# Optimization experiments

Hardware: AMD Instinct MI355X
Metric: run time of the kernel (lower is better)

The kernel has to match this reference:

```python
import jax, jax.numpy as jnp
import numpy as np

MARGIN = 0.5
AP_VALUE = 0.8
AN_VALUE = 0.4
ABS_W = 1.0


def setup_inputs() -> dict:
    key = jax.random.key(0)
    k1, k2 = jax.random.split(key)
    bs, d = 16384, 64
    inputs = jax.random.normal(k1, (bs, d), dtype=jnp.float32)
    target = jax.random.randint(k2, (bs,), 0, 64, dtype=jnp.int64)
    return {"inputs": inputs, "target": target}


def reference(inputs, target):
    # L2-normalize features (normalize_feature=True)
    x = inputs / jnp.linalg.norm(inputs, axis=-1, keepdims=True)

    # cross-entropy on normalized features treated as logits
    logp = jax.nn.log_softmax(x, axis=-1)  # [bs, d]
    loss_ce = -jnp.mean(jnp.take_along_axis(logp, target[:, None], axis=1))

    # cosine-similarity matrix [bs, bs]
    dist = x @ x.T

    is_pos = target[None, :] == target[:, None]
    # hard mining: min similarity among positives, max among negatives (per row)
    dist_ap = jnp.min(jnp.where(is_pos, dist, jnp.inf), axis=1)   # [bs]
    dist_an = jnp.max(jnp.where(is_pos, -jnp.inf, dist), axis=1)  # [bs]

    loss = jnp.mean(jax.nn.relu(MARGIN + dist_ap - dist_an))

    # absolute (angular margin) terms
    abs_ap = jax.nn.relu(AP_VALUE - dist_ap)
    abs_an = jax.nn.relu(dist_an - AN_VALUE)
    loss = (jnp.mean(abs_an) + jnp.mean(abs_ap)) * ABS_W + loss

    return loss + loss_ce
```

## Files before the change

kernel.cpp:

```cpp
#include <hip/hip_runtime.h>


#define N_ROWS 16384
#define N_DIM 64

typedef __attribute__((ext_vector_type(8))) short bf16x8;
typedef __attribute__((ext_vector_type(4))) float f32x4;

__device__ inline unsigned short f2bf(float f) {
  unsigned u = __float_as_uint(f);
  unsigned r = u + 0x7fffu + ((u >> 16) & 1u);
  return (unsigned short)(r >> 16);
}

__device__ inline unsigned enc_key(float f) {
  unsigned u = __float_as_uint(f);
  return (u & 0x80000000u) ? ~u : (u | 0x80000000u);
}
__device__ inline float dec_key(unsigned k) {
  unsigned u = (k & 0x80000000u) ? (k ^ 0x80000000u) : ~k;
  return __uint_as_float(u);
}

__global__ void perm_kernel(const int* __restrict__ tgt, int* __restrict__ perm,
                            int* __restrict__ ts, int* __restrict__ class_start,
                            unsigned* __restrict__ mp_key, unsigned* __restrict__ mn_key) {
  __shared__ int hist[64];
  __shared__ int start[65];
  __shared__ int cursor[64];
  const int tid = threadIdx.x;
  if (tid < 64) hist[tid] = 0;
  for (int i = tid; i < N_ROWS; i += 1024) { mp_key[i] = 0xFFFFFFFFu; mn_key[i] = 0u; }
  __syncthreads();
  int c[16];
#pragma unroll
  for (int k = 0; k < 16; ++k) {
    c[k] = tgt[tid + k * 1024];
    atomicAdd(&hist[c[k]], 1);
  }
  __syncthreads();
  if (tid < 64) {
    int s = 0;
    for (int j = 0; j < tid; ++j) s += hist[j];
    start[tid] = s; cursor[tid] = s; class_start[tid] = s;
    if (tid == 63) { start[64] = s + hist[63]; class_start[64] = s + hist[63]; }
  }
  __syncthreads();
#pragma unroll
  for (int k = 0; k < 16; ++k) {
    const int r = tid + k * 1024;
    const int pos = atomicAdd(&cursor[c[k]], 1);
    perm[r] = pos;
    ts[pos] = c[k];
  }
}

__global__ void prep_kernel(const float* __restrict__ x, const int* __restrict__ tgt,
                            const int* __restrict__ perm,
                            unsigned short* __restrict__ xs, float* __restrict__ ce_row) {
  const int row  = blockIdx.x * 4 + (threadIdx.x >> 6);
  const int lane = threadIdx.x & 63;
  float v  = x[row * N_DIM + lane];
  float ss = v * v;
#pragma unroll
  for (int s = 1; s < 64; s <<= 1) ss += __shfl_xor(ss, s, 64);
  float xn = v * rsqrtf(ss);
  xs[perm[row] * N_DIM + lane] = f2bf(xn);

  float mx = xn;
#pragma unroll
  for (int s = 1; s < 64; s <<= 1) mx = fmaxf(mx, __shfl_xor(mx, s, 64));
  float e  = __expf(xn - mx);
  float se = e;
#pragma unroll
  for (int s = 1; s < 64; s <<= 1) se += __shfl_xor(se, s, 64);
  float lse = mx + __logf(se);
  int   t   = tgt[row];
  float xt  = __shfl(xn, t, 64);
  if (lane == 0) ce_row[row] = lse - xt;
}

__global__ void mine_kernel(const unsigned short* __restrict__ xs, const int* __restrict__ ts,
                            const int* __restrict__ class_start,
                            unsigned* __restrict__ mp_key, unsigned* __restrict__ mn_key) {
  const int lane    = threadIdx.x & 63;
  const int wv      = threadIdx.x >> 6;
  const int iblk    = blockIdx.x >> 5;
  const int jspl    = blockIdx.x & 31;
  const int rowbase = iblk * 256 + wv * 64;
  const int m = lane & 15, q = lane >> 4;

  bf16x8 a[4][2];
#pragma unroll
  for (int tr = 0; tr < 4; ++tr) {
    const unsigned short* p = xs + (rowbase + tr * 16 + m) * N_DIM + q * 8;
    a[tr][0] = *(const bf16x8*)(p);
    a[tr][1] = *(const bf16x8*)(p + 32);
  }
  int ti[4][4];
#pragma unroll
  for (int tr = 0; tr < 4; ++tr)
#pragma unroll
    for (int r = 0; r < 4; ++r)
      ti[tr][r] = ts[rowbase + tr * 16 + q * 4 + r];

  const int cmin = ts[rowbase];
  const int cmax = ts[rowbase + 63];
  const int lo   = class_start[cmin];
  const int hi   = class_start[cmax + 1];

  float mp[16], mn[16];
#pragma unroll
  for (int k = 0; k < 16; ++k) { mp[k] = __builtin_inff(); mn[k] = -__builtin_inff(); }

  const int jbase = jspl * 512;

  const unsigned short* p0 = xs + (jbase + m) * N_DIM + q * 8;
  bf16x8 b0 = *(const bf16x8*)p0;
  bf16x8 b1 = *(const bf16x8*)(p0 + 32);

  for (int jc = 0; jc < 32; ++jc) {
    bf16x8 cb0 = b0, cb1 = b1;
    const int jb = jbase + jc * 16;
    if (jc < 31) {
      const unsigned short* np = xs + (jb + 16 + m) * N_DIM + q * 8;
      b0 = *(const bf16x8*)np;
      b1 = *(const bf16x8*)(np + 32);
    }
    const bool slow = (jb < hi) && (jb + 16 > lo);
    if (slow) {
      const int ctj = ts[jb + m];
#pragma unroll
      for (int tr = 0; tr < 4; ++tr) {
        f32x4 acc = {0.f, 0.f, 0.f, 0.f};
        acc = __builtin_amdgcn_mfma_f32_16x16x32_bf16(a[tr][0], cb0, acc, 0, 0, 0);
        acc = __builtin_amdgcn_mfma_f32_16x16x32_bf16(a[tr][1], cb1, acc, 0, 0, 0);
#pragma unroll
        for (int r = 0; r < 4; ++r) {
          const bool  pos = (ctj == ti[tr][r]);
          const float d   = acc[r];
          const int   k   = tr * 4 + r;
          mp[k] = fminf(mp[k], pos ? d : __builtin_inff());
          mn[k] = fmaxf(mn[k], pos ? -__builtin_inff() : d);
        }
      }
    } else {
#pragma unroll
      for (int tr = 0; tr < 4; ++tr) {
        f32x4 acc = {0.f, 0.f, 0.f, 0.f};
        acc = __builtin_amdgcn_mfma_f32_16x16x32_bf16(a[tr][0], cb0, acc, 0, 0, 0);
        acc = __builtin_amdgcn_mfma_f32_16x16x32_bf16(a[tr][1], cb1, acc, 0, 0, 0);
#pragma unroll
        for (int r = 0; r < 4; ++r)
          mn[tr * 4 + r] = fmaxf(mn[tr * 4 + r], acc[r]);
      }
    }
  }

#pragma unroll
  for (int s = 1; s < 16; s <<= 1) {
#pragma unroll
    for (int k = 0; k < 16; ++k) {
      mp[k] = fminf(mp[k], __shfl_xor(mp[k], s, 64));
      mn[k] = fmaxf(mn[k], __shfl_xor(mn[k], s, 64));
    }
  }
  if (m == 0) {
#pragma unroll
    for (int tr = 0; tr < 4; ++tr)
#pragma unroll
      for (int r = 0; r < 4; ++r) {
        const int row = rowbase + tr * 16 + q * 4 + r;
        atomicMin(&mp_key[row], enc_key(mp[tr * 4 + r]));
        atomicMax(&mn_key[row], enc_key(mn[tr * 4 + r]));
      }
  }
}

__global__ void finalize_kernel(const unsigned* __restrict__ mp_key, const unsigned* __restrict__ mn_key,
                                const float* __restrict__ ce_row, float* __restrict__ out) {
  __shared__ float red[4][16];
  float s1 = 0.f, s2 = 0.f, s3 = 0.f, s4 = 0.f;
  for (int r = threadIdx.x; r < N_ROWS; r += 1024) {
    float ap = dec_key(mp_key[r]);
    float an = dec_key(mn_key[r]);
    s1 += fmaxf(0.5f + ap - an, 0.f);
    s2 += fmaxf(0.8f - ap, 0.f);
    s3 += fmaxf(an - 0.4f, 0.f);
    s4 += ce_row[r];
  }
#pragma unroll
  for (int s = 1; s < 64; s <<= 1) {
    s1 += __shfl_xor(s1, s, 64);
    s2 += __shfl_xor(s2, s, 64);
    s3 += __shfl_xor(s3, s, 64);
    s4 += __shfl_xor(s4, s, 64);
  }
  const int wv = threadIdx.x >> 6;
  if ((threadIdx.x & 63) == 0) {
    red[0][wv] = s1; red[1][wv] = s2; red[2][wv] = s3; red[3][wv] = s4;
  }
  __syncthreads();
  if (threadIdx.x == 0) {
    float t = 0.f;
#pragma unroll
    for (int c = 0; c < 4; ++c) {
      float tc = 0.f;
#pragma unroll
      for (int w = 0; w < 16; ++w) tc += red[c][w];
      t += tc;
    }
    out[0] = t * (1.0f / N_ROWS);
  }
}

extern "C" void kernel_launch(void* const* d_in, const int* in_sizes, int n_in,
                              void* d_out, int out_size, void* d_ws, size_t ws_size,
                              hipStream_t stream) {
  const float* x   = (const float*)d_in[0];
  const int*   tgt = (const int*)d_in[1];
  char* ws = (char*)d_ws;

  unsigned short* xs     = (unsigned short*)ws;
  unsigned*       mp_key = (unsigned*)(ws + (2u << 20));
  unsigned*       mn_key = (unsigned*)(ws + (2u << 20) + (64u << 10));
  float*          ce_row = (float*)(ws + (2u << 20) + (128u << 10));
  int*            perm   = (int*)(ws + (2u << 20) + (192u << 10));
  int*            ts     = (int*)(ws + (2u << 20) + (256u << 10));
  int*            cstart = (int*)(ws + (2u << 20) + (320u << 10));
  float*          out    = (float*)d_out;

  perm_kernel<<<1, 1024, 0, stream>>>(tgt, perm, ts, cstart, mp_key, mn_key);
  prep_kernel<<<N_ROWS / 4, 256, 0, stream>>>(x, tgt, perm, xs, ce_row);
  mine_kernel<<<64 * 32, 256, 0, stream>>>(xs, ts, cstart, mp_key, mn_key);
  finalize_kernel<<<1, 1024, 0, stream>>>(mp_key, mn_key, ce_row, out);
}
```

Measured before the change: 167.8 us.

## Parallelize class sort across blocks and widen mining column tiles

Replaces the single-block perm kernel with separate init, multi-block histogram, wave-scan and multi-block scatter kernels, so the sorting preprocessing runs over more of the GPU. The mining kernel now uses 16 column splits of 1024 columns each and loads four 16-column B tiles per iteration to expose more independent MFMAs and loads. It also adds launch bounds hinting three blocks per SM. The cost is three extra kernel launches and fewer mining blocks (1024 instead of 2048), which could leave CUs underused. The scatter order within a class is nondeterministic across blocks, but only the class grouping matters for correctness.

```diff
diff --git a/kernel.cpp b/kernel.cpp
--- a/kernel.cpp
+++ b/kernel.cpp
@@ -22,37 +22,45 @@
   return __uint_as_float(u);
 }
 
-__global__ void perm_kernel(const int* __restrict__ tgt, int* __restrict__ perm,
-                            int* __restrict__ ts, int* __restrict__ class_start,
-                            unsigned* __restrict__ mp_key, unsigned* __restrict__ mn_key) {
-  __shared__ int hist[64];
-  __shared__ int start[65];
-  __shared__ int cursor[64];
+__global__ void init_kernel(unsigned* __restrict__ mp_key, unsigned* __restrict__ mn_key,
+                            int* __restrict__ hist) {
+  const int i = blockIdx.x * 256 + threadIdx.x;
+  mp_key[i] = 0xFFFFFFFFu;
+  mn_key[i] = 0u;
+  if (blockIdx.x == 0 && threadIdx.x < 64) hist[threadIdx.x] = 0;
+}
+
+__global__ void hist_kernel(const int* __restrict__ tgt, int* __restrict__ hist) {
+  __shared__ int h[64];
+  if (threadIdx.x < 64) h[threadIdx.x] = 0;
+  __syncthreads();
+  atomicAdd(&h[tgt[blockIdx.x * 1024 + threadIdx.x]], 1);
+  __syncthreads();
+  if (threadIdx.x < 64) atomicAdd(&hist[threadIdx.x], h[threadIdx.x]);
+}
+
+__global__ void scan_kernel(const int* __restrict__ hist, int* __restrict__ class_start,
+                            int* __restrict__ cursor) {
   const int tid = threadIdx.x;
-  if (tid < 64) hist[tid] = 0;
-  for (int i = tid; i < N_ROWS; i += 1024) { mp_key[i] = 0xFFFFFFFFu; mn_key[i] = 0u; }
-  __syncthreads();
-  int c[16];
-#pragma unroll
-  for (int k = 0; k < 16; ++k) {
-    c[k] = tgt[tid + k * 1024];
-    atomicAdd(&hist[c[k]], 1);
-  }
-  __syncthreads();
-  if (tid < 64) {
-    int s = 0;
-    for (int j = 0; j < tid; ++j) s += hist[j];
-    start[tid] = s; cursor[tid] = s; class_start[tid] = s;
-    if (tid == 63) { start[64] = s + hist[63]; class_start[64] = s + hist[63]; }
-  }
-  __syncthreads();
-#pragma unroll
-  for (int k = 0; k < 16; ++k) {
-    const int r = tid + k * 1024;
-    const int pos = atomicAdd(&cursor[c[k]], 1);
-    perm[r] = pos;
-    ts[pos] = c[k];
-  }
+  const int h = hist[tid];
+  int s = h;
+#pragma unroll
+  for (int d = 1; d < 64; d <<= 1) {
+    int t = __shfl_up(s, d, 64);
+    if (tid >= d) s += t;
+  }
+  class_start[tid] = s - h;
+  cursor[tid]      = s - h;
+  if (tid == 63) class_start[64] = s;
+}
+
+__global__ void scatter_kernel(const int* __restrict__ tgt, int* __restrict__ cursor,
+                               int* __restrict__ perm, int* __restrict__ ts) {
+  const int r = blockIdx.x * 1024 + threadIdx.x;
+  const int c = tgt[r];
+  const int pos = atomicAdd(&cursor[c], 1);
+  perm[r] = pos;
+  ts[pos] = c;
 }
 
 __global__ void prep_kernel(const float* __restrict__ x, const int* __restrict__ tgt,
@@ -80,13 +88,14 @@
   if (lane == 0) ce_row[row] = lse - xt;
 }
 
-__global__ void mine_kernel(const unsigned short* __restrict__ xs, const int* __restrict__ ts,
-                            const int* __restrict__ class_start,
-                            unsigned* __restrict__ mp_key, unsigned* __restrict__ mn_key) {
+__global__ void __launch_bounds__(256, 3)
+mine_kernel(const unsigned short* __restrict__ xs, const int* __restrict__ ts,
+            const int* __restrict__ class_start,
+            unsigned* __restrict__ mp_key, unsigned* __restrict__ mn_key) {
   const int lane    = threadIdx.x & 63;
   const int wv      = threadIdx.x >> 6;
-  const int iblk    = blockIdx.x >> 5;
-  const int jspl    = blockIdx.x & 31;
+  const int iblk    = blockIdx.x >> 4;
+  const int jspl    = blockIdx.x & 15;
   const int rowbase = iblk * 256 + wv * 64;
   const int m = lane & 15, q = lane >> 4;
 
@@ -97,62 +106,60 @@
     a[tr][0] = *(const bf16x8*)(p);
     a[tr][1] = *(const bf16x8*)(p + 32);
   }
-  int ti[4][4];
+  int ti[16];
 #pragma unroll
   for (int tr = 0; tr < 4; ++tr)
 #pragma unroll
     for (int r = 0; r < 4; ++r)
-      ti[tr][r] = ts[rowbase + tr * 16 + q * 4 + r];
-
-  const int cmin = ts[rowbase];
-  const int cmax = ts[rowbase + 63];
-  const int lo   = class_start[cmin];
-  const int hi   = class_start[cmax + 1];
+      ti[tr * 4 + r] = ts[rowbase + tr * 16 + q * 4 + r];
+
+  const int lo = class_start[ts[rowbase]];
+  const int hi = class_start[ts[rowbase + 63] + 1];
 
   float mp[16], mn[16];
 #pragma unroll
   for (int k = 0; k < 16; ++k) { mp[k] = __builtin_inff(); mn[k] = -__builtin_inff(); }
 
-  const int jbase = jspl * 512;
-
-  const unsigned short* p0 = xs + (jbase + m) * N_DIM + q * 8;
-  bf16x8 b0 = *(const bf16x8*)p0;
-  bf16x8 b1 = *(const bf16x8*)(p0 + 32);
-
-  for (int jc = 0; jc < 32; ++jc) {
-    bf16x8 cb0 = b0, cb1 = b1;
-    const int jb = jbase + jc * 16;
-    if (jc < 31) {
-      const unsigned short* np = xs + (jb + 16 + m) * N_DIM + q * 8;
-      b0 = *(const bf16x8*)np;
-      b1 = *(const bf16x8*)(np + 32);
+  const int jbase = jspl * 1024;
+  const unsigned short* pw = xs + jbase * N_DIM;
+  const int loff = m * N_DIM + q * 8;
+  const f32x4 fz = {0.f, 0.f, 0.f, 0.f};
+
+  for (int it = 0; it < 16; ++it) {
+    const unsigned short* p = pw + it * (64 * N_DIM) + loff;
+    bf16x8 b[4][2];
+#pragma unroll
+    for (int tc = 0; tc < 4; ++tc) {
+      b[tc][0] = *(const bf16x8*)(p + tc * (16 * N_DIM));
+      b[tc][1] = *(const bf16x8*)(p + tc * (16 * N_DIM) + 32);
     }
-    const bool slow = (jb < hi) && (jb + 16 > lo);
-    if (slow) {
-      const int ctj = ts[jb + m];
-#pragma unroll
-      for (int tr = 0; tr < 4; ++tr) {
-        f32x4 acc = {0.f, 0.f, 0.f, 0.f};
-        acc = __builtin_amdgcn_mfma_f32_16x16x32_bf16(a[tr][0], cb0, acc, 0, 0, 0);
-        acc = __builtin_amdgcn_mfma_f32_16x16x32_bf16(a[tr][1], cb1, acc, 0, 0, 0);
-#pragma unroll
-        for (int r = 0; r < 4; ++r) {
-          const bool  pos = (ctj == ti[tr][r]);
-          const float d   = acc[r];
-          const int   k   = tr * 4 + r;
-          mp[k] = fminf(mp[k], pos ? d : __builtin_inff());
-          mn[k] = fmaxf(mn[k], pos ? -__builtin_inff() : d);
+    const int jb0 = jbase + it * 64;
+#pragma unroll
+    for (int tc = 0; tc < 4; ++tc) {
+      const int jb = jb0 + tc * 16;
+      if ((jb < hi) && (jb + 16 > lo)) {
+        const int ctj = ts[jb + m];
+#pragma unroll
+        for (int tr = 0; tr < 4; ++tr) {
+          f32x4 acc = __builtin_amdgcn_mfma_f32_16x16x32_bf16(a[tr][0], b[tc][0], fz, 0, 0, 0);
+          acc = __builtin_amdgcn_mfma_f32_16x16x32_bf16(a[tr][1], b[tc][1], acc, 0, 0, 0);
+#pragma unroll
+          for (int r = 0; r < 4; ++r) {
+            const bool  pos = (ctj == ti[tr * 4 + r]);
+            const float d   = acc[r];
+            mp[tr * 4 + r] = fminf(mp[tr * 4 + r], pos ? d : __builtin_inff());
+            mn[tr * 4 + r] = fmaxf(mn[tr * 4 + r], pos ? -__builtin_inff() : d);
+          }
         }
-      }
-    } else {
-#pragma unroll
-      for (int tr = 0; tr < 4; ++tr) {
-        f32x4 acc = {0.f, 0.f, 0.f, 0.f};
-        acc = __builtin_amdgcn_mfma_f32_16x16x32_bf16(a[tr][0], cb0, acc, 0, 0, 0);
-        acc = __builtin_amdgcn_mfma_f32_16x16x32_bf16(a[tr][1], cb1, acc, 0, 0, 0);
-#pragma unroll
-        for (int r = 0; r < 4; ++r)
-          mn[tr * 4 + r] = fmaxf(mn[tr * 4 + r], acc[r]);
+      } else {
+#pragma unroll
+        for (int tr = 0; tr < 4; ++tr) {
+          f32x4 acc = __builtin_amdgcn_mfma_f32_16x16x32_bf16(a[tr][0], b[tc][0], fz, 0, 0, 0);
+          acc = __builtin_amdgcn_mfma_f32_16x16x32_bf16(a[tr][1], b[tc][1], acc, 0, 0, 0);
+#pragma unroll
+          for (int r = 0; r < 4; ++r)
+            mn[tr * 4 + r] = fmaxf(mn[tr * 4 + r], acc[r]);
+        }
       }
     }
   }
@@ -204,12 +211,9 @@
   if (threadIdx.x == 0) {
     float t = 0.f;
 #pragma unroll
-    for (int c = 0; c < 4; ++c) {
-      float tc = 0.f;
-#pragma unroll
-      for (int w = 0; w < 16; ++w) tc += red[c][w];
-      t += tc;
-    }
+    for (int c = 0; c < 4; ++c)
+#pragma unroll
+      for (int w = 0; w < 16; ++w) t += red[c][w];
     out[0] = t * (1.0f / N_ROWS);
   }
 }
@@ -228,10 +232,15 @@
   int*            perm   = (int*)(ws + (2u << 20) + (192u << 10));
   int*            ts     = (int*)(ws + (2u << 20) + (256u << 10));
   int*            cstart = (int*)(ws + (2u << 20) + (320u << 10));
+  int*            hist   = (int*)(ws + (2u << 20) + (321u << 10));
+  int*            cursor = (int*)(ws + (2u << 20) + (322u << 10));
   float*          out    = (float*)d_out;
 
-  perm_kernel<<<1, 1024, 0, stream>>>(tgt, perm, ts, cstart, mp_key, mn_key);
+  init_kernel<<<64, 256, 0, stream>>>(mp_key, mn_key, hist);
+  hist_kernel<<<16, 1024, 0, stream>>>(tgt, hist);
+  scan_kernel<<<1, 64, 0, stream>>>(hist, cstart, cursor);
+  scatter_kernel<<<16, 1024, 0, stream>>>(tgt, cursor, perm, ts);
   prep_kernel<<<N_ROWS / 4, 256, 0, stream>>>(x, tgt, perm, xs, ce_row);
-  mine_kernel<<<64 * 32, 256, 0, stream>>>(xs, ts, cstart, mp_key, mn_key);
+  mine_kernel<<<64 * 16, 256, 0, stream>>>(xs, ts, cstart, mp_key, mn_key);
   finalize_kernel<<<1, 1024, 0, stream>>>(mp_key, mn_key, ce_row, out);
 }
```

Result: slower. 184.9 us (+10.2%).
